# Kernel tuning notes

Measured on AMD Instinct MI355X. Metric: run time of the kernel, lower is better.

Reference implementation:

```python
import jax, jax.numpy as jnp
import numpy as np

B, M, N, C, L = 4, 500, 500, 91, 3


def _lsa(cost):
    """Exact linear sum assignment (shortest augmenting path / LAPJV),
    numpy port of scipy's rectangular_lsap for a square cost matrix.
    Returns col4row: col4row[i] = column assigned to row i."""
    n = cost.shape[0]
    u = np.zeros(n, dtype=np.float64)
    v = np.zeros(n, dtype=np.float64)
    col4row = np.full(n, -1, dtype=np.int64)
    row4col = np.full(n, -1, dtype=np.int64)
    cost = cost.astype(np.float64)
    for cur_row in range(n):
        min_val = 0.0
        i = cur_row
        remaining = np.ones(n, dtype=bool)
        shortest = np.full(n, np.inf)
        path = np.full(n, -1, dtype=np.int64)
        SR = []
        sink = -1
        while sink == -1:
            SR.append(i)
            r = min_val + cost[i] - u[i] - v
            better = remaining & (r < shortest)
            shortest = np.where(better, r, shortest)
            path = np.where(better, i, path)
            masked = np.where(remaining, shortest, np.inf)
            j = int(np.argmin(masked))
            min_val = masked[j]
            remaining[j] = False
            if row4col[j] == -1:
                sink = j
            else:
                i = int(row4col[j])
        u[cur_row] += min_val
        sr = np.array(SR[1:], dtype=np.int64)
        if sr.size:
            u[sr] += min_val - shortest[col4row[sr]]
        scanned_cols = ~remaining
        v[scanned_cols] -= min_val - shortest[scanned_cols]
        # augment along the alternating path
        j = sink
        while True:
            i = int(path[j])
            row4col[j] = i
            col4row[i], j = j, col4row[i]
            if i == cur_row:
                break
    return col4row


def _assignment(cost_np):
    """(B, M, N) numpy cost -> (B, M) row->col mapping (square => all assigned)."""
    return np.stack([_lsa(c) for c in cost_np]).astype(np.int64)


def _cost_matrix(p2_boxes, p2_logits, p1_boxes, p1_logits):
    # center L2 distance: cdist(boxes2[..., :2], boxes1[..., :2], p=2) -> (B, M, N)
    diff = p2_boxes[:, :, None, :2] - p1_boxes[:, None, :, :2]
    center_d = jnp.sqrt(jnp.sum(diff * diff, axis=-1))
    # class disparity: cdist(sigmoid(l2), sigmoid(l1), p=inf) -> (B, M, N)
    s2 = jax.nn.sigmoid(p2_logits)
    s1 = jax.nn.sigmoid(p1_logits)
    class_d = jnp.max(jnp.abs(s2[:, :, None, :] - s1[:, None, :, :]), axis=-1)
    return 0.5 * center_d + 0.5 * class_d


def _extrapolate(p2_boxes, p2_logits, p1_boxes, p1_logits, mapping, factor):
    has = mapping != -1                      # (B, M)
    m = jnp.where(has, mapping, 0)
    idx4 = jnp.broadcast_to(m[:, :, None], m.shape + (4,))
    corr_b1 = jnp.take_along_axis(p1_boxes, idx4, axis=1)
    corr_b1 = jnp.where(has[:, :, None], corr_b1, p2_boxes)
    # 'linear' dim extrapolation, clamped at 0
    pos = p2_boxes[..., 0:2] + (p2_boxes[..., 0:2] - corr_b1[..., 0:2]) * factor
    dim = jnp.maximum(p2_boxes[..., 2:4] + (p2_boxes[..., 2:4] - corr_b1[..., 2:4]) * factor, 0.0)
    boxes3 = jnp.concatenate([pos, dim], axis=2)
    nclass = p1_logits.shape[-1]
    idxc = jnp.broadcast_to(m[:, :, None], m.shape + (nclass,))
    corr_l1 = jnp.take_along_axis(p1_logits, idxc, axis=1)
    corr_l1 = jnp.where(has[:, :, None], corr_l1, 0.0)
    logits3 = 0.5 * (p2_logits + corr_l1)
    return boxes3, logits3


def setup_inputs() -> dict:
    key = jax.random.key(0)
    k1, k2, k3, k4, k5 = jax.random.split(key, 5)
    pred1_boxes = jax.random.uniform(k1, (B, N, 4), dtype=jnp.float32)
    pred1_logits = jax.random.normal(k2, (B, N, C), dtype=jnp.float32)
    pred2_boxes = jax.random.uniform(k3, (B, M, 4), dtype=jnp.float32)
    pred2_logits = jax.random.normal(k4, (B, M, C), dtype=jnp.float32)
    # strictly increasing timestamps so offsets are positive
    temporal_offsets = jnp.cumsum(
        jax.random.uniform(k5, (B, L), minval=0.1, maxval=1.0, dtype=jnp.float32), axis=1)
    return {
        "pred1_boxes": pred1_boxes,
        "pred1_logits": pred1_logits,
        "pred2_boxes": pred2_boxes,
        "pred2_logits": pred2_logits,
        "temporal_offsets": temporal_offsets,
    }


def reference(pred1_boxes, pred1_logits, pred2_boxes, pred2_logits, temporal_offsets):
    cost = _cost_matrix(pred2_boxes, pred2_logits, pred1_boxes, pred1_logits)
    mapping = jnp.asarray(_assignment(np.asarray(cost)))  # (B, M) int64
    first = temporal_offsets[:, 1] - temporal_offsets[:, 0]
    second = temporal_offsets[:, 2] - temporal_offsets[:, 1]
    factor = (second / first)[:, None, None]
    boxes3, logits3 = _extrapolate(pred2_boxes, pred2_logits,
                                   pred1_boxes, pred1_logits, mapping, factor)
    return boxes3, logits3
```

## Files before the change

kernel.cpp:

```cpp
#include <hip/hip_runtime.h>
#include <math.h>

#define Bq 4
#define Mq 500
#define Nq 500
#define Cq 91
#define NPHASE 5
#define KEEP_TOL 1e-6f

__device__ __forceinline__ float sigmoidf_(float x) {
    return 1.0f / (1.0f + expf(-x));
}

__global__ __launch_bounds__(256) void cost_kernel(
    const float* __restrict__ p1_boxes, const float* __restrict__ p1_logits,
    const float* __restrict__ p2_boxes, const float* __restrict__ p2_logits,
    float* __restrict__ cost)
{
    __shared__ float s2t[16][Cq + 1];
    __shared__ float s1t[16][Cq + 1];
    __shared__ float b2x[16], b2y[16], b1x[16], b1y[16];
    const int b  = blockIdx.z;
    const int i0 = blockIdx.y * 16;
    const int j0 = blockIdx.x * 16;
    const int tid = threadIdx.x;

    for (int t = tid; t < 16 * Cq; t += 256) {
        const int r = t / Cq, c = t - r * Cq;
        const int i = min(i0 + r, Mq - 1);
        const int j = min(j0 + r, Nq - 1);
        s2t[r][c] = sigmoidf_(p2_logits[((size_t)b * Mq + i) * Cq + c]);
        s1t[r][c] = sigmoidf_(p1_logits[((size_t)b * Nq + j) * Cq + c]);
    }
    if (tid < 16) {
        const int i = min(i0 + tid, Mq - 1);
        const int j = min(j0 + tid, Nq - 1);
        b2x[tid] = p2_boxes[((size_t)b * Mq + i) * 4 + 0];
        b2y[tid] = p2_boxes[((size_t)b * Mq + i) * 4 + 1];
        b1x[tid] = p1_boxes[((size_t)b * Nq + j) * 4 + 0];
        b1y[tid] = p1_boxes[((size_t)b * Nq + j) * 4 + 1];
    }
    __syncthreads();

    const int ty = tid >> 4, tx = tid & 15;
    const int i = i0 + ty, j = j0 + tx;
    if (i < Mq && j < Nq) {
        float mx = 0.0f;
        #pragma unroll 7
        for (int c = 0; c < Cq; ++c)
            mx = fmaxf(mx, fabsf(s2t[ty][c] - s1t[tx][c]));
        const float dx = b2x[ty] - b1x[tx];
        const float dy = b2y[ty] - b1y[tx];
        const float cd = sqrtf(dx * dx + dy * dy);
        cost[((size_t)b * Mq + i) * Nq + j] = 0.5f * cd + 0.5f * mx;
    }
}

__global__ __launch_bounds__(256) void colred_kernel(
    const float* __restrict__ cost, float* __restrict__ v0, int* __restrict__ amin)
{
    const int j = blockIdx.x * 256 + threadIdx.x;
    const int b = blockIdx.y;
    if (j >= Nq) return;
    const float* __restrict__ cb = cost + (size_t)b * Mq * Nq;
    float best = INFINITY;
    int bi = 0;
    #pragma unroll 4
    for (int i = 0; i < Mq; ++i) {
        const float c = cb[(size_t)i * Nq + j];
        if (c < best) { best = c; bi = i; }
    }
    v0[b * Nq + j] = best;
    amin[b * Nq + j] = bi;
}

template<int CTRL>
__device__ __forceinline__ float dppminv_(float x) {
    const int moved = __builtin_amdgcn_update_dpp(
        0x7F800000, __float_as_int(x), CTRL, 0xF, 0xF, false);
    return fminf(x, __int_as_float(moved));
}
__device__ __forceinline__ float wave_min_f32_(float x) {
    x = dppminv_<0x111>(x);
    x = dppminv_<0x112>(x);
    x = dppminv_<0x114>(x);
    x = dppminv_<0x118>(x);
    x = dppminv_<0x142>(x);
    x = dppminv_<0x143>(x);
    return __int_as_float(__builtin_amdgcn_readlane(__float_as_int(x), 63));
}

__device__ __forceinline__ void pairmin_(float& va, unsigned& pa, float vb, unsigned pb) {
    const bool le = (va <= vb);
    va = fminf(va, vb);
    pa = le ? pa : pb;
}

__device__ __forceinline__ unsigned long long pack_bid_(float p, int row) {
    return ((unsigned long long)__float_as_uint(p) << 32) | (unsigned)(row + 1);
}

__global__ __launch_bounds__(1024) void auction_kernel(
    const float* __restrict__ cost, const float* __restrict__ v0,
    const int* __restrict__ amin,
    float* __restrict__ v_out, int* __restrict__ owner_out)
{
    constexpr int n = Nq;
    __shared__ float p_lds[512];
    __shared__ int   owner_lds[512];
    __shared__ int   match_lds[512];
    __shared__ unsigned long long bid_lds[512];
    __shared__ int   flist[512];
    __shared__ int   jlist[512];
    __shared__ int   nfree_lds, njl_lds;

    const float eps_tab[NPHASE] = {4e-3f, 8e-4f, 1.6e-4f, 3.2e-5f, 0.0f};
    const int   cap_tab[NPHASE] = {48, 32, 32, 32, 64};

    const int tid = threadIdx.x;
    const int lane = tid & 63;
    const int wv = tid >> 6;
    const int b = blockIdx.x;
    const float* __restrict__ cb = cost + (size_t)b * n * n;

    const unsigned init_mask = (lane < 61) ? 0xFFu : 0x0Fu;
    const int off2 = (lane < 61) ? 256 + 4 * lane : 0;

    float v0_r[8];
    {
        const float4 a0 = *(const float4*)(v0 + b * n + 4 * lane);
        const float4 a1 = *(const float4*)(v0 + b * n + off2);
        const float vv[8] = {a0.x, a0.y, a0.z, a0.w, a1.x, a1.y, a1.z, a1.w};
        #pragma unroll
        for (int k = 0; k < 8; ++k)
            v0_r[k] = ((init_mask >> k) & 1) ? vv[k] : 0.0f;
    }
    if (tid < 512) {
        p_lds[tid] = 0.0f; owner_lds[tid] = -1; match_lds[tid] = -1;
        bid_lds[tid] = 0ull;
    }
    __syncthreads();
    if (tid < n) {
        const int i0 = amin[b * n + tid];
        if (atomicCAS(&match_lds[i0], -1, tid) == -1) owner_lds[tid] = i0;
    }
    __syncthreads();

    for (int ph = 0; ph < NPHASE; ++ph) {
        const float eps = eps_tab[ph];
        const int cap = cap_tab[ph];
        if (ph > 0) {
            if (tid < 512) { owner_lds[tid] = -1; match_lds[tid] = -1; }
        }
        __syncthreads();

        for (int round = 0; round < cap; ++round) {
            if (tid == 0) { nfree_lds = 0; njl_lds = 0; }
            __syncthreads();
            if (tid < n && match_lds[tid] < 0)
                flist[atomicAdd(&nfree_lds, 1)] = tid;
            __syncthreads();
            const int nf = nfree_lds;
            if (nf == 0) break;

            for (int idx = wv; idx < nf; idx += 16) {
                const int i = flist[idx];
                const float* __restrict__ crow = cb + (size_t)i * n;
                const float4 c0 = *(const float4*)(crow + 4 * lane);
                const float4 c1 = *(const float4*)(crow + off2);
                const float4 p0 = *(const float4*)&p_lds[4 * lane];
                const float4 p1 = *(const float4*)&p_lds[off2];
                const float cc[8] = {c0.x, c0.y, c0.z, c0.w, c1.x, c1.y, c1.z, c1.w};
                const float pp[8] = {p0.x, p0.y, p0.z, p0.w, p1.x, p1.y, p1.z, p1.w};
                float d[8]; unsigned pj[8];
                #pragma unroll
                for (int k = 0; k < 8; ++k) {
                    const int j = (k < 4) ? 4 * lane + k : 256 + 4 * lane + (k - 4);
                    d[k] = ((init_mask >> k) & 1) ? cc[k] - v0_r[k] + pp[k] : INFINITY;
                    pj[k] = (unsigned)j;
                }
                float    a0 = d[0], a1 = d[1], a2 = d[2], a3 = d[3];
                float    a4 = d[4], a5 = d[5], a6 = d[6], a7 = d[7];
                unsigned b0 = pj[0], b1 = pj[1], b2 = pj[2], b3 = pj[3];
                unsigned b4 = pj[4], b5 = pj[5], b6 = pj[6], b7 = pj[7];
                pairmin_(a0, b0, a1, b1);  pairmin_(a2, b2, a3, b3);
                pairmin_(a4, b4, a5, b5);  pairmin_(a6, b6, a7, b7);
                pairmin_(a0, b0, a2, b2);  pairmin_(a4, b4, a6, b6);
                pairmin_(a0, b0, a4, b4);
                const float lmin = a0;
                const unsigned lpay = b0;

                const float g1 = wave_min_f32_(lmin);
                const unsigned long long cm = __ballot(lmin == g1);
                const int wl = (int)__builtin_ctzll(cm);
                const int j1 = __builtin_amdgcn_readlane((int)lpay, wl);

                const int ow = (j1 >> 2) & 63, kw = ((j1 >> 8) << 2) | (j1 & 3);
                float lmin2 = INFINITY;
                #pragma unroll
                for (int k = 0; k < 8; ++k) {
                    const float dv = (k == kw && lane == ow) ? INFINITY : d[k];
                    lmin2 = fminf(lmin2, dv);
                }
                const float g2 = wave_min_f32_(lmin2);

                if (lane == 0) {
                    const float pnew = p_lds[j1] + (g2 - g1) + eps;
                    atomicMax(&bid_lds[j1], pack_bid_(pnew, i));
                    jlist[atomicAdd(&njl_lds, 1)] = j1;
                }
            }
            __syncthreads();

            const int nj = njl_lds;
            for (int t = tid; t < nj; t += 1024) {
                const int j = jlist[t];
                const unsigned long long bd = atomicExch(&bid_lds[j], 0ull);
                if (bd != 0ull) {
                    const int ri = (int)(bd & 0xFFFFFFFFull) - 1;
                    const float pn = __uint_as_float((unsigned)(bd >> 32));
                    const int prev = owner_lds[j];
                    if (prev >= 0) match_lds[prev] = -1;
                    owner_lds[j] = ri;
                    match_lds[ri] = j;
                    p_lds[j] = pn;
                }
            }
            __syncthreads();
        }
    }

    if (tid < n) {
        v_out[b * n + tid] = v0[b * n + tid] - p_lds[tid];
        owner_out[b * n + tid] = owner_lds[tid];
    }
}

__global__ __launch_bounds__(64) void lsa_kernel(
    const float* __restrict__ cost, const float* __restrict__ v_in,
    const int* __restrict__ owner_in, int* __restrict__ mapping)
{
    constexpr int n = Nq;
    __shared__ float u_lds[512];
    __shared__ float shortest_lds[512];
    __shared__ int   path_lds[512];
    __shared__ int   row4col_lds[512];
    __shared__ int   col4row_lds[512];
    __shared__ int   fr_lds[512];
    __shared__ int   nfr_lds;

    const int lane = threadIdx.x;
    const int b = blockIdx.x;
    const float* __restrict__ cb = cost + (size_t)b * n * n;

    const unsigned init_mask = (lane < 61) ? 0xFFu : 0x0Fu;
    const int off2 = (lane < 61) ? 256 + 4 * lane : 0;

    float v_r[8], vwork_r[8], short_r[8], shortfin_r[8], t_r[8];
    int path_r[8];
    unsigned pay_r[8];

    {
        const float4 a0 = *(const float4*)(v_in + b * n + 4 * lane);
        const float4 a1 = *(const float4*)(v_in + b * n + off2);
        const float vv[8] = {a0.x, a0.y, a0.z, a0.w, a1.x, a1.y, a1.z, a1.w};
        #pragma unroll
        for (int k = 0; k < 8; ++k)
            v_r[k] = ((init_mask >> k) & 1) ? vv[k] : 0.0f;
    }
    for (int t = lane; t < 512; t += 64) {
        u_lds[t] = 0.0f; row4col_lds[t] = -1; col4row_lds[t] = -1;
    }
    __syncthreads();
    for (int t = lane; t < n; t += 64) {
        const int r = owner_in[b * n + t];
        if (r >= 0 && atomicCAS(&col4row_lds[r], -1, t) == -1)
            row4col_lds[t] = r;
    }
    __syncthreads();

    {
        int j1c = col4row_lds[0];
        float4 ta0 = *(const float4*)(cb + 4 * lane);
        float4 ta1 = *(const float4*)(cb + off2);
        for (int i2 = 0; i2 < n; ++i2) {
            const float4 c0 = ta0, c1 = ta1;
            const int j1 = j1c;
            const int inx = (i2 + 1 < n) ? i2 + 1 : i2;
            const float* __restrict__ crn = cb + (size_t)inx * n;
            ta0 = *(const float4*)(crn + 4 * lane);
            ta1 = *(const float4*)(crn + off2);
            j1c = col4row_lds[inx];
            if (j1 < 0) continue;
            const float cc[8] = {c0.x, c0.y, c0.z, c0.w, c1.x, c1.y, c1.z, c1.w};
            const int owner = (j1 >> 2) & 63;
            const int kwin  = ((j1 >> 8) << 2) | (j1 & 3);
            float d[8];
            float rcj = INFINITY;
            #pragma unroll
            for (int k = 0; k < 8; ++k) {
                const bool mine = (k == kwin && lane == owner);
                const bool use = ((init_mask >> k) & 1) && !mine;
                d[k] = use ? cc[k] - v_r[k] : INFINITY;
                if (mine) rcj = cc[k] - v_r[k];
            }
            const float mu = wave_min_f32_(
                fminf(fminf(fminf(d[0], d[1]), fminf(d[2], d[3])),
                      fminf(fminf(d[4], d[5]), fminf(d[6], d[7]))));
            const float rc1g = __int_as_float(
                __builtin_amdgcn_readlane(__float_as_int(rcj), owner));
            const bool keep = (rc1g <= mu + KEEP_TOL);
            #pragma unroll
            for (int k = 0; k < 8; ++k)
                if (keep && k == kwin && lane == owner)
                    v_r[k] = fminf(v_r[k], cc[k] - mu);
            if (lane == 0) {
                if (keep) u_lds[i2] = mu;
                else { row4col_lds[j1] = -1; col4row_lds[i2] = -1; }
            }
        }
    }
    __syncthreads();

    if (lane == 0) nfr_lds = 0;
    __syncthreads();
    for (int t = lane; t < n; t += 64)
        if (col4row_lds[t] < 0) fr_lds[atomicAdd(&nfr_lds, 1)] = t;
    __syncthreads();

    for (int aug = 0; aug < n; ++aug) {
        const int nfr = nfr_lds;
        if (nfr == 0) break;

        {
            const int4 r0 = *(const int4*)&row4col_lds[4 * lane];
            const int4 r1 = *(const int4*)&row4col_lds[off2];
            const int rr[8] = {r0.x, r0.y, r0.z, r0.w, r1.x, r1.y, r1.z, r1.w};
            #pragma unroll
            for (int k = 0; k < 8; ++k) {
                const int j = (k < 4) ? 4 * lane + k : 256 + 4 * lane + (k - 4);
                const bool valid = (init_mask >> k) & 1;
                pay_r[k] = valid ? (((unsigned)j << 10) | (unsigned)(rr[k] + 1))
                                 : 0xFFFFFFFFu;
                vwork_r[k] = valid ? v_r[k] : -INFINITY;
                short_r[k] = INFINITY;
                shortfin_r[k] = INFINITY;
                path_r[k] = -1;
            }
        }

        {
            int fi = fr_lds[0];
            const float* __restrict__ crow = cb + (size_t)fi * n;
            float4 s0 = *(const float4*)(crow + 4 * lane);
            float4 s1 = *(const float4*)(crow + off2);
            for (int t = 0; t < nfr; ++t) {
                const float4 c0 = s0, c1 = s1;
                const int cur_fi = fi;
                const int tn = (t + 1 < nfr) ? t + 1 : t;
                fi = fr_lds[tn];
                const float* __restrict__ crn = cb + (size_t)fi * n;
                s0 = *(const float4*)(crn + 4 * lane);
                s1 = *(const float4*)(crn + off2);
                const float a = -u_lds[cur_fi];
                #pragma unroll
                for (int k = 0; k < 8; ++k) t_r[k] = a - vwork_r[k];
                const float cvk[8] = {c0.x, c0.y, c0.z, c0.w,
                                      c1.x, c1.y, c1.z, c1.w};
                #pragma unroll
                for (int k = 0; k < 8; ++k) {
                    const float r = cvk[k] + t_r[k];
                    if (r < short_r[k]) { short_r[k] = r; path_r[k] = cur_fi; }
                }
            }
        }

        int sink_j = -1;
        float min_val = 0.0f;
        unsigned sr_mask = 0;
        bool have_cv = false;
        float4 cv0, cv1;
        float a = 0.0f;
        int i_cur = -1;

        for (int pops = 0; pops <= n; ++pops) {
            if (have_cv) {
                #pragma unroll
                for (int k = 0; k < 8; ++k) t_r[k] = a - vwork_r[k];
                {
                    const float c4[4] = {cv0.x, cv0.y, cv0.z, cv0.w};
                    #pragma unroll
                    for (int k = 0; k < 4; ++k) {
                        const float r = c4[k] + t_r[k];
                        if (r < short_r[k]) { short_r[k] = r; path_r[k] = i_cur; }
                    }
                }
                {
                    const float c4[4] = {cv1.x, cv1.y, cv1.z, cv1.w};
                    #pragma unroll
                    for (int k = 0; k < 4; ++k) {
                        const float r = c4[k] + t_r[4 + k];
                        if (r < short_r[4 + k]) { short_r[4 + k] = r; path_r[4 + k] = i_cur; }
                    }
                }
            }

            float    m0 = short_r[0], m1 = short_r[1], m2 = short_r[2], m3 = short_r[3];
            float    m4 = short_r[4], m5 = short_r[5], m6 = short_r[6], m7 = short_r[7];
            unsigned q0 = pay_r[0], q1 = pay_r[1], q2 = pay_r[2], q3 = pay_r[3];
            unsigned q4 = pay_r[4], q5 = pay_r[5], q6 = pay_r[6], q7 = pay_r[7];
            pairmin_(m0, q0, m1, q1);  pairmin_(m2, q2, m3, q3);
            pairmin_(m4, q4, m5, q5);  pairmin_(m6, q6, m7, q7);
            pairmin_(m0, q0, m2, q2);  pairmin_(m4, q4, m6, q6);
            pairmin_(m0, q0, m4, q4);
            const float lmin = m0;
            const unsigned lpay = q0;

            const float gmin = wave_min_f32_(lmin);
            const unsigned long long cand = __ballot(lmin == gmin);
            const int wl = (int)__builtin_ctzll(cand);
            const unsigned win = (unsigned)__builtin_amdgcn_readlane((int)lpay, wl);

            min_val = gmin;
            const unsigned jst = win >> 10;
            const unsigned rc1 = win & 0x3FFu;

            const int i_next = (int)rc1 - 1;
            const int i_safe = (i_next < 0) ? 0 : i_next;
            const float* __restrict__ crow2 = cb + (size_t)i_safe * n;
            cv0 = *(const float4*)(crow2 + 4 * lane);
            cv1 = *(const float4*)(crow2 + off2);
            a = gmin - u_lds[i_safe];

            const int owner = (int)((jst >> 2) & 63u);
            const int kwin  = (int)(((jst >> 8) << 2) | (jst & 3u));
            #pragma unroll
            for (int k = 0; k < 8; ++k) {
                if (k == kwin && lane == owner) {
                    shortfin_r[k] = short_r[k];
                    short_r[k] = INFINITY;
                    vwork_r[k] = -INFINITY;
                }
            }

            if (rc1 == 0u) { sink_j = (int)jst; break; }
            if ((i_next & 63) == lane) sr_mask |= 1u << (i_next >> 6);
            i_cur = i_next;
            have_cv = true;
        }

        if (sink_j < 0) break;

        *(float4*)&shortest_lds[4 * lane] =
            make_float4(shortfin_r[0], shortfin_r[1], shortfin_r[2], shortfin_r[3]);
        *(int4*)&path_lds[4 * lane] =
            make_int4(path_r[0], path_r[1], path_r[2], path_r[3]);
        *(float4*)&shortest_lds[256 + 4 * lane] =
            make_float4(shortfin_r[4], shortfin_r[5], shortfin_r[6], shortfin_r[7]);
        *(int4*)&path_lds[256 + 4 * lane] =
            make_int4(path_r[4], path_r[5], path_r[6], path_r[7]);
        __syncthreads();

        #pragma unroll
        for (int k = 0; k < 8; ++k) {
            const int t = lane + (k << 6);
            if (t < n && (sr_mask & (1u << k)))
                u_lds[t] += min_val - shortest_lds[col4row_lds[t]];
        }
        for (int t = lane; t < nfr; t += 64)
            u_lds[fr_lds[t]] += min_val;
        #pragma unroll
        for (int k = 0; k < 8; ++k) {
            if (((init_mask >> k) & 1) && vwork_r[k] == -INFINITY)
                v_r[k] -= min_val - shortfin_r[k];
        }
        __syncthreads();

        if (lane == 0) {
            int j = sink_j;
            int origin = -1;
            for (;;) {
                const int ii = path_lds[j];
                row4col_lds[j] = ii;
                const int tmp = col4row_lds[ii];
                col4row_lds[ii] = j;
                if (tmp < 0) { origin = ii; break; }
                j = tmp;
            }
            const int m = nfr_lds;
            for (int t = 0; t < m; ++t) {
                if (fr_lds[t] == origin) {
                    fr_lds[t] = fr_lds[m - 1];
                    break;
                }
            }
            nfr_lds = m - 1;
        }
        __syncthreads();
    }

    for (int t = lane; t < n; t += 64)
        mapping[b * n + t] = col4row_lds[t];
}

__global__ __launch_bounds__(256) void extrap_boxes_kernel(
    const float* __restrict__ p1_boxes, const float* __restrict__ p2_boxes,
    const float* __restrict__ toffs, const int* __restrict__ mapping,
    float* __restrict__ out_boxes)
{
    const int idx = blockIdx.x * blockDim.x + threadIdx.x;
    if (idx >= Bq * Mq) return;
    const int b = idx / Mq;
    const float t0 = toffs[b * 3 + 0], t1 = toffs[b * 3 + 1], t2 = toffs[b * 3 + 2];
    const float factor = (t2 - t1) / (t1 - t0);
    const int m = mapping[idx];
    const float4 p2 = ((const float4*)p2_boxes)[idx];
    const float4 p1 = (m >= 0) ? ((const float4*)p1_boxes)[b * Nq + m] : p2;
    float4 o;
    o.x = p2.x + (p2.x - p1.x) * factor;
    o.y = p2.y + (p2.y - p1.y) * factor;
    o.z = fmaxf(p2.z + (p2.z - p1.z) * factor, 0.0f);
    o.w = fmaxf(p2.w + (p2.w - p1.w) * factor, 0.0f);
    ((float4*)out_boxes)[idx] = o;
}

__global__ __launch_bounds__(256) void extrap_logits_kernel(
    const float* __restrict__ p1_logits, const float* __restrict__ p2_logits,
    const int* __restrict__ mapping, float* __restrict__ out_logits)
{
    const int idx = blockIdx.x * blockDim.x + threadIdx.x;
    if (idx >= Bq * Mq * Cq) return;
    const int c = idx % Cq;
    const int bi = idx / Cq;
    const int b = bi / Mq;
    const int m = mapping[bi];
    const float corr = (m >= 0) ? p1_logits[((size_t)b * Nq + m) * Cq + c] : 0.0f;
    out_logits[idx] = 0.5f * (p2_logits[idx] + corr);
}

extern "C" void kernel_launch(void* const* d_in, const int* in_sizes, int n_in,
                              void* d_out, int out_size, void* d_ws, size_t ws_size,
                              hipStream_t stream) {
    const float* p1_boxes  = (const float*)d_in[0];
    const float* p1_logits = (const float*)d_in[1];
    const float* p2_boxes  = (const float*)d_in[2];
    const float* p2_logits = (const float*)d_in[3];
    const float* toffs     = (const float*)d_in[4];
    float* out = (float*)d_out;

    char* ws = (char*)d_ws;
    float* cost    = (float*)ws;
    int*   mapping = (int*)  (ws + 4000000);
    float* v0      = (float*)(ws + 4008000);
    int*   amin    = (int*)  (ws + 4016000);
    float* v_auc   = (float*)(ws + 4024000);
    int*   owner   = (int*)  (ws + 4032000);

    dim3 cgrid((Nq + 15) / 16, (Mq + 15) / 16, Bq);
    cost_kernel<<<cgrid, 256, 0, stream>>>(p1_boxes, p1_logits, p2_boxes, p2_logits, cost);

    colred_kernel<<<dim3(2, Bq), 256, 0, stream>>>(cost, v0, amin);

    auction_kernel<<<Bq, 1024, 0, stream>>>(cost, v0, amin, v_auc, owner);

    lsa_kernel<<<Bq, 64, 0, stream>>>(cost, v_auc, owner, mapping);

    extrap_boxes_kernel<<<(Bq * Mq + 255) / 256, 256, 0, stream>>>(
        p1_boxes, p2_boxes, toffs, mapping, out);
    extrap_logits_kernel<<<(Bq * Mq * Cq + 255) / 256, 256, 0, stream>>>(
        p1_logits, p2_logits, mapping, out + Bq * Mq * 4);
}
```

Before: 1.901 ms.

## Batch-pop all near-minimum columns per Dijkstra step in LSA augmentation

Replaces the one-column-at-a-time shortest-path pop in the LSA kernel with a batched step: every remaining column whose tentative distance is within a small tolerance of the wave minimum is popped together, unless it is a free sink, and its owning row is then relaxed in a pipelined loop. This aims to cut the number of serialized wave-reduction iterations per augmentation. In exchange it adds LDS atomics and two barriers per iteration. The tolerance-based batching can also change tie-breaking and slightly alter the order of relaxation compared with the exact one-at-a-time algorithm.

```diff
diff --git a/kernel.cpp b/kernel.cpp
--- a/kernel.cpp
+++ b/kernel.cpp
@@ -7,6 +7,7 @@
 #define Cq 91
 #define NPHASE 5
 #define KEEP_TOL 1e-6f
+#define BATCH_TAU 1e-6f
 
 __device__ __forceinline__ float sigmoidf_(float x) {
     return 1.0f / (1.0f + expf(-x));
@@ -247,7 +248,9 @@
     __shared__ int   row4col_lds[512];
     __shared__ int   col4row_lds[512];
     __shared__ int   fr_lds[512];
-    __shared__ int   nfr_lds;
+    __shared__ int   brow_lds[512];
+    __shared__ float bdist_lds[512];
+    __shared__ int   nfr_lds, nb_lds;
 
     const int lane = threadIdx.x;
     const int b = blockIdx.x;
@@ -378,33 +381,8 @@
         int sink_j = -1;
         float min_val = 0.0f;
         unsigned sr_mask = 0;
-        bool have_cv = false;
-        float4 cv0, cv1;
-        float a = 0.0f;
-        int i_cur = -1;
-
-        for (int pops = 0; pops <= n; ++pops) {
-            if (have_cv) {
-                #pragma unroll
-                for (int k = 0; k < 8; ++k) t_r[k] = a - vwork_r[k];
-                {
-                    const float c4[4] = {cv0.x, cv0.y, cv0.z, cv0.w};
-                    #pragma unroll
-                    for (int k = 0; k < 4; ++k) {
-                        const float r = c4[k] + t_r[k];
-                        if (r < short_r[k]) { short_r[k] = r; path_r[k] = i_cur; }
-                    }
-                }
-                {
-                    const float c4[4] = {cv1.x, cv1.y, cv1.z, cv1.w};
-                    #pragma unroll
-                    for (int k = 0; k < 4; ++k) {
-                        const float r = c4[k] + t_r[4 + k];
-                        if (r < short_r[4 + k]) { short_r[4 + k] = r; path_r[4 + k] = i_cur; }
-                    }
-                }
-            }
-
+
+        for (int iter = 0; iter <= n; ++iter) {
             float    m0 = short_r[0], m1 = short_r[1], m2 = short_r[2], m3 = short_r[3];
             float    m4 = short_r[4], m5 = short_r[5], m6 = short_r[6], m7 = short_r[7];
             unsigned q0 = pay_r[0], q1 = pay_r[1], q2 = pay_r[2], q3 = pay_r[3];
@@ -424,29 +402,55 @@
             min_val = gmin;
             const unsigned jst = win >> 10;
             const unsigned rc1 = win & 0x3FFu;
-
-            const int i_next = (int)rc1 - 1;
-            const int i_safe = (i_next < 0) ? 0 : i_next;
-            const float* __restrict__ crow2 = cb + (size_t)i_safe * n;
-            cv0 = *(const float4*)(crow2 + 4 * lane);
-            cv1 = *(const float4*)(crow2 + off2);
-            a = gmin - u_lds[i_safe];
-
-            const int owner = (int)((jst >> 2) & 63u);
-            const int kwin  = (int)(((jst >> 8) << 2) | (jst & 3u));
+            if (rc1 == 0u) { sink_j = (int)jst; break; }
+
+            if (lane == 0) nb_lds = 0;
+            __syncthreads();
+            const float thr = gmin + BATCH_TAU;
             #pragma unroll
             for (int k = 0; k < 8; ++k) {
-                if (k == kwin && lane == owner) {
-                    shortfin_r[k] = short_r[k];
-                    short_r[k] = INFINITY;
-                    vwork_r[k] = -INFINITY;
-                }
-            }
-
-            if (rc1 == 0u) { sink_j = (int)jst; break; }
-            if ((i_next & 63) == lane) sr_mask |= 1u << (i_next >> 6);
-            i_cur = i_next;
-            have_cv = true;
+                if (short_r[k] <= thr) {
+                    const unsigned rc = pay_r[k] & 0x3FFu;
+                    if (rc != 0u) {
+                        const int bi = atomicAdd(&nb_lds, 1);
+                        brow_lds[bi] = (int)rc - 1;
+                        bdist_lds[bi] = short_r[k];
+                        shortfin_r[k] = short_r[k];
+                        short_r[k] = INFINITY;
+                        vwork_r[k] = -INFINITY;
+                    }
+                }
+            }
+            __syncthreads();
+            const int K = nb_lds;
+
+            {
+                int rr = brow_lds[0];
+                const float* __restrict__ crow = cb + (size_t)rr * n;
+                float4 s0 = *(const float4*)(crow + 4 * lane);
+                float4 s1 = *(const float4*)(crow + off2);
+                for (int t = 0; t < K; ++t) {
+                    const float4 c0 = s0, c1 = s1;
+                    const int cr = rr;
+                    const float dist = bdist_lds[t];
+                    const int tn = (t + 1 < K) ? t + 1 : t;
+                    rr = brow_lds[tn];
+                    const float* __restrict__ crn = cb + (size_t)rr * n;
+                    s0 = *(const float4*)(crn + 4 * lane);
+                    s1 = *(const float4*)(crn + off2);
+                    if ((cr & 63) == lane) sr_mask |= 1u << (cr >> 6);
+                    const float a2 = dist - u_lds[cr];
+                    #pragma unroll
+                    for (int k = 0; k < 8; ++k) t_r[k] = a2 - vwork_r[k];
+                    const float cvk[8] = {c0.x, c0.y, c0.z, c0.w,
+                                          c1.x, c1.y, c1.z, c1.w};
+                    #pragma unroll
+                    for (int k = 0; k < 8; ++k) {
+                        const float r = cvk[k] + t_r[k];
+                        if (r < short_r[k]) { short_r[k] = r; path_r[k] = cr; }
+                    }
+                }
+            }
         }
 
         if (sink_j < 0) break;
```

Result: slower. 1.979 ms (+4.1%).
